# Kernel optimization log

Hardware: AMD Instinct MI355X
Metric: run time of the kernel (lower is better)

Reference implementation:

```python
import jax, jax.numpy as jnp
import numpy as np

N, E, B = 200000, 1600000, 4096
IN_FEATS, H, R, NB = 64, 32, 8, 2


def _params(key):
    ks = jax.random.split(key, 20)
    p = {}
    dims = [(IN_FEATS, H), (H, H), (H, H), (H, H)]
    i = 0
    for l, (di, do) in enumerate(dims):
        p[f'basis{l}'] = jax.random.normal(ks[i], (NB, di, do), jnp.float32) * 0.1; i += 1
        p[f'comp{l}'] = jax.random.normal(ks[i], (R, NB), jnp.float32) * 0.1; i += 1
        p[f'wself{l}'] = jax.random.normal(ks[i], (di, do), jnp.float32) * 0.1; i += 1
        p[f'bias{l}'] = jnp.zeros((do,), jnp.float32); i += 1
    p['lin1_w'] = jax.random.normal(ks[i], (2 * 4 * H, 1), jnp.float32) * 0.05; i += 1
    p['lin1_b'] = jnp.zeros((1,), jnp.float32)
    return p


def setup_inputs() -> dict:
    key = jax.random.key(0)
    k = jax.random.split(key, 8)
    inp = {
        'x': jax.random.normal(k[0], (N, IN_FEATS), jnp.float32),
        'src': jax.random.randint(k[1], (E,), 0, N, jnp.int32),
        'dst': jax.random.randint(k[2], (E,), 0, N, jnp.int32),
        'etype': jax.random.randint(k[3], (E,), 0, R, jnp.int32),
        'user_idx': jax.random.randint(k[4], (B,), 0, N, jnp.int32),
        'item_idx': jax.random.randint(k[5], (B,), 0, N, jnp.int32),
    }
    inp.update(_params(k[6]))
    return inp


def _rel_graph_conv(x, src, dst, etype, basis, comp, wself, bias):
    # basis decomposition: W_r = sum_b comp[r,b] * basis[b]
    # compute per-node per-basis transform first (cheap: small NB), then mix per edge
    hb = jnp.einsum('ni,bio->nbo', x, basis)            # [N, NB, out]
    msg = jnp.einsum('eb,ebo->eo', comp[etype], hb[src])  # [E, out]
    agg = jax.ops.segment_sum(msg, dst, num_segments=x.shape[0])
    return agg + x @ wself + bias


def reference(x, src, dst, etype, user_idx, item_idx,
              basis0, comp0, wself0, bias0,
              basis1, comp1, wself1, bias1,
              basis2, comp2, wself2, bias2,
              basis3, comp3, wself3, bias3,
              lin1_w, lin1_b):
    states = []
    h = x
    for (ba, co, ws, bi) in ((basis0, comp0, wself0, bias0),
                             (basis1, comp1, wself1, bias1),
                             (basis2, comp2, wself2, bias2),
                             (basis3, comp3, wself3, bias3)):
        h = jnp.tanh(_rel_graph_conv(h, src, dst, etype, ba, co, ws, bi))
        states.append(h)
    cat = jnp.concatenate(states, axis=1)               # [N, 128]
    pair = jnp.concatenate([cat[user_idx], cat[item_idx]], axis=1)  # [B, 256]
    out = jax.nn.sigmoid(pair @ lin1_w + lin1_b)        # [B, 1]
    return out[:, 0]  # multiply_by == 1
```

## Files before the change

kernel.cpp:

```cpp
#include <hip/hip_runtime.h>
#include <hip/hip_bf16.h>


#define SRC_MASK 0x3FFFFu
#define BUK_SH 9
#define BUK_W 512

typedef __attribute__((ext_vector_type(8))) short bf16x8;
typedef __attribute__((ext_vector_type(4))) float f32x4;
typedef unsigned short u16;
typedef unsigned int u32;

__device__ inline u32 f2bf(float f) {
    u32 u = __float_as_uint(f);
    return (u + 0x7FFFu + ((u >> 16) & 1u)) >> 16;
}
__device__ inline float bf2f(u32 lo16) { return __uint_as_float(lo16 << 16); }

__device__ inline float fast_tanh(float x) {
    float xc = fminf(fmaxf(x, -15.f), 15.f);
    float e = __expf(2.f * xc);
    return (e - 1.f) * __builtin_amdgcn_rcpf(e + 1.f);
}

__device__ inline void block_exscan(int* a, int M, int* wsum ) {
    const int t = threadIdx.x;
    const int q = M >> 2;
    int s0 = 0, s1 = 0, s2 = 0, s3 = 0, s = 0;
    if (t < q) {
        s0 = a[4 * t]; s1 = a[4 * t + 1]; s2 = a[4 * t + 2]; s3 = a[4 * t + 3];
        s = s0 + s1 + s2 + s3;
    }
    int lane = t & 63, wid = t >> 6;
    int val = s;
    for (int d = 1; d < 64; d <<= 1) {
        int u = __shfl_up(val, d, 64);
        if (lane >= d) val += u;
    }
    if (lane == 63) wsum[wid] = val;
    __syncthreads();
    int woff = 0;
    for (int w = 0; w < wid; ++w) woff += wsum[w];
    val += woff;
    int base = val - s;
    __syncthreads();
    if (t < q) {
        a[4 * t]     = base;
        a[4 * t + 1] = base + s0;
        a[4 * t + 2] = base + s0 + s1;
        a[4 * t + 3] = base + s0 + s1 + s2;
    }
    __syncthreads();
}

__global__ __launch_bounds__(256) void k_buk_count(const int* __restrict__ dst,
                                                   int* __restrict__ gBukCnt, int E) {
    __shared__ int hist[1024];
    const int t = threadIdx.x;
    for (int f = t; f < 1024; f += 256) hist[f] = 0;
    __syncthreads();
    int e0 = blockIdx.x * 2048;
    for (int k = 0; k < 8; ++k) {
        int e = e0 + k * 256 + t;
        if (e < E) atomicAdd(&hist[dst[e] >> BUK_SH], 1);
    }
    __syncthreads();
    for (int f = t; f < 1024; f += 256) {
        int c = hist[f];
        if (c) atomicAdd(&gBukCnt[f], c);
    }
}

__global__ void k_buk_scan(const int* __restrict__ gBukCnt, int* __restrict__ bukOff,
                           int nb) {
    __shared__ int lds[1024];
    int tid = threadIdx.x;
    int v = (tid < nb) ? gBukCnt[tid] : 0;
    lds[tid] = v;
    __syncthreads();
    for (int d = 1; d < 1024; d <<= 1) {
        int u = (tid >= d) ? lds[tid - d] : 0;
        __syncthreads();
        lds[tid] += u;
        __syncthreads();
    }
    if (tid < nb) bukOff[tid] = lds[tid] - v;
    if (tid == nb - 1) bukOff[nb] = lds[tid];
}

__global__ __launch_bounds__(256) void k_binscatter(
    const int* __restrict__ src, const int* __restrict__ dst,
    const int* __restrict__ etype, const int* __restrict__ bukOff,
    int* __restrict__ gBukCur, unsigned int* __restrict__ binned,
    int E, int NBUK)
{
    __shared__ int hist[1024];
    __shared__ int offs[1024];
    __shared__ int cur[1024];
    __shared__ int gb[1024];
    __shared__ int wsum[4];
    __shared__ unsigned int stage[2048];
    __shared__ unsigned short stageB[2048];
    const int t = threadIdx.x;
    for (int f = t; f < 1024; f += 256) { hist[f] = 0; cur[f] = 0; }
    __syncthreads();

    const int e0 = blockIdx.x * 2048;
    const int cntTot = min(2048, E - e0);
    unsigned int pk[8];
    int bk[8];
#pragma unroll
    for (int k = 0; k < 8; ++k) {
        int e = e0 + k * 256 + t;
        if (e < E) {
            int d = dst[e];
            bk[k] = d >> BUK_SH;
            pk[k] = (unsigned int)src[e]
                  | ((unsigned int)etype[e] << 29)
                  | ((unsigned int)(d & (BUK_W - 1)) << 20);
            atomicAdd(&hist[bk[k]], 1);
        } else bk[k] = -1;
    }
    __syncthreads();
    for (int f = t; f < 1024; f += 256) offs[f] = hist[f];
    __syncthreads();
    block_exscan(offs, 1024, wsum);
#pragma unroll
    for (int k = 0; k < 8; ++k) {
        if (bk[k] >= 0) {
            int pos = offs[bk[k]] + atomicAdd(&cur[bk[k]], 1);
            stage[pos] = pk[k];
            stageB[pos] = (unsigned short)bk[k];
        }
    }
    for (int f = t; f < NBUK; f += 256) {
        int c = hist[f];
        if (c > 0) gb[f] = bukOff[f] + atomicAdd(&gBukCur[f], c);
    }
    __syncthreads();
    for (int k = t; k < cntTot; k += 256) {
        int b = stageB[k];
        binned[(size_t)gb[b] + (size_t)(k - offs[b])] = stage[k];
    }
}

__global__ __launch_bounds__(256) void k_bucket_finalize(
    const unsigned int* __restrict__ binned, const int* __restrict__ bukOff,
    int* __restrict__ rowptr, unsigned int* __restrict__ epack, int N, int E)
{
    __shared__ int nhist[512];
    __shared__ int ncur[512];
    __shared__ int wsum[4];
    const int t = threadIdx.x;
    const int b = blockIdx.x;
    for (int f = t; f < 512; f += 256) { nhist[f] = 0; ncur[f] = 0; }
    __syncthreads();
    const int k0 = bukOff[b], k1 = bukOff[b + 1];
    for (int k = k0 + t; k < k1; k += 256)
        atomicAdd(&nhist[(binned[k] >> 20) & (BUK_W - 1)], 1);
    __syncthreads();
    block_exscan(nhist, 512, wsum);
    for (int f = t; f < 512; f += 256) {
        int node = (b << BUK_SH) + f;
        if (node < N) rowptr[node] = k0 + nhist[f];
    }
    if (b == 0 && t == 0) rowptr[N] = E;
    for (int k = k0 + t; k < k1; k += 256) {
        unsigned int v = binned[k];
        int dl = (v >> 20) & (BUK_W - 1);
        int pos = k0 + nhist[dl] + atomicAdd(&ncur[dl], 1);
        epack[pos] = v & 0xE003FFFFu;
    }
}

template<int DI>
__global__ __launch_bounds__(256) void k_transform3(
    const float* __restrict__ xin, int in_stride,
    const float* __restrict__ basis, const float* __restrict__ wself,
    const float* __restrict__ bias,
    u32* __restrict__ hb2, float* __restrict__ self0, int n)
{
    constexpr int ROWB = DI * 2;
    constexpr int SMASK = (ROWB / 16) - 1;
    constexpr int C4 = DI / 4;
    __shared__ u16 xs[64 * DI];
    __shared__ u16 bt[96 * DI];
    const int t = threadIdx.x;

    auto swz = [](int row, int byteInRow) -> int {
        int slot = (byteInRow >> 4) ^ ((row ^ (row >> 2)) & SMASK);
        return row * ROWB + (slot << 4) + (byteInRow & 15);
    };

    for (int f = t; f < 96 * C4; f += 256) {
        int k4 = f / 96;
        int o  = f - k4 * 96;
        const float* sp = (o < 64) ? (basis + (size_t)(o >> 5) * DI * 32 + (o & 31))
                                   : (wself + (o - 64));
        int k = 4 * k4;
        ushort4 pv;
        pv.x = (u16)f2bf(sp[(size_t)(k + 0) * 32]);
        pv.y = (u16)f2bf(sp[(size_t)(k + 1) * 32]);
        pv.z = (u16)f2bf(sp[(size_t)(k + 2) * 32]);
        pv.w = (u16)f2bf(sp[(size_t)(k + 3) * 32]);
        *(ushort4*)((char*)bt + swz(o, k * 2)) = pv;
    }

    const int node0 = blockIdx.x * 64;
    for (int f = t; f < 64 * C4; f += 256) {
        int nloc = f / C4, k4 = f - nloc * C4;
        int node = node0 + nloc;
        float4 v = make_float4(0.f, 0.f, 0.f, 0.f);
        if (node < n) v = *(const float4*)(xin + (size_t)node * in_stride + 4 * k4);
        ushort4 pv;
        pv.x = (u16)f2bf(v.x);
        pv.y = (u16)f2bf(v.y);
        pv.z = (u16)f2bf(v.z);
        pv.w = (u16)f2bf(v.w);
        *(ushort4*)((char*)xs + swz(nloc, 8 * k4)) = pv;
    }
    __syncthreads();

    const int w = t >> 6;
    const int l = t & 63;
    const int lr = l & 15;
    const int lg = l >> 4;

    f32x4 c[6];
#pragma unroll
    for (int i = 0; i < 6; ++i) c[i] = (f32x4){0.f, 0.f, 0.f, 0.f};

#pragma unroll
    for (int ks = 0; ks < DI / 32; ++ks) {
        const int kb = ks * 64 + lg * 16;
        bf16x8 a = *(const bf16x8*)((char*)xs + swz(w * 16 + lr, kb));
#pragma unroll
        for (int tt = 0; tt < 6; ++tt) {
            bf16x8 b = *(const bf16x8*)((char*)bt + swz(tt * 16 + lr, kb));
            c[tt] = __builtin_amdgcn_mfma_f32_16x16x32_bf16(a, b, c[tt], 0, 0, 0);
        }
    }

    const float bia0 = bias[lr];
    const float bia1 = bias[16 + lr];
#pragma unroll
    for (int r = 0; r < 4; ++r) {
        int node = node0 + w * 16 + lg * 4 + r;
        if (node < n) {
            hb2[(size_t)node * 32 + lr]      = f2bf(c[0][r]) | (f2bf(c[2][r]) << 16);
            hb2[(size_t)node * 32 + 16 + lr] = f2bf(c[1][r]) | (f2bf(c[3][r]) << 16);
            self0[(size_t)node * 32 + lr]      = c[4][r] + bia0;
            self0[(size_t)node * 32 + 16 + lr] = c[5][r] + bia1;
        }
    }
}

template<int W>
__device__ __forceinline__ void agg0_block(
    const u32* __restrict__ hb2, const u32* __restrict__ epack,
    int k, int oj, unsigned gbase, const u32* cw, float4& acc)
{
    int pa;
    if (W == 8)      pa = (int)epack[k + oj];
    else if (W == 4) pa = (int)epack[k + (oj & 3)];
    else if (W == 2) pa = (int)epack[k + (oj & 1)];
    else             pa = (int)epack[k];
    u32 pp[W];
    uint4 hh[W];
#pragma unroll
    for (int j = 0; j < W; ++j) {
        pp[j] = (W > 1) ? (u32)__shfl(pa, j, 8) : (u32)pa;
        unsigned boff = (pp[j] & SRC_MASK) * 128u + gbase;
        hh[j] = *(const uint4*)((const char*)hb2 + boff);
    }
#pragma unroll
    for (int j = 0; j < W; ++j) {
        u32 w = cw[pp[j] >> 29];
        float w0 = __uint_as_float(w << 16);
        float w1 = __uint_as_float(w & 0xFFFF0000u);
        acc.x = fmaf(w0, __uint_as_float(hh[j].x << 16), acc.x);
        acc.x = fmaf(w1, __uint_as_float(hh[j].x & 0xFFFF0000u), acc.x);
        acc.y = fmaf(w0, __uint_as_float(hh[j].y << 16), acc.y);
        acc.y = fmaf(w1, __uint_as_float(hh[j].y & 0xFFFF0000u), acc.y);
        acc.z = fmaf(w0, __uint_as_float(hh[j].z << 16), acc.z);
        acc.z = fmaf(w1, __uint_as_float(hh[j].z & 0xFFFF0000u), acc.z);
        acc.w = fmaf(w0, __uint_as_float(hh[j].w << 16), acc.w);
        acc.w = fmaf(w1, __uint_as_float(hh[j].w & 0xFFFF0000u), acc.w);
    }
}

__global__ __launch_bounds__(256) void k_aggregate0(
    const u32* __restrict__ hb2,
    const u32* __restrict__ epack,
    const int* __restrict__ rowptr,
    const float* __restrict__ comp,
    const float* __restrict__ self0,
    u16* __restrict__ cat0,
    int n)
{
    __shared__ u32 cw[8];
    if (threadIdx.x < 8)
        cw[threadIdx.x] = f2bf(comp[threadIdx.x * 2 + 0])
                        | (f2bf(comp[threadIdx.x * 2 + 1]) << 16);
    __syncthreads();
    int t = blockIdx.x * 256 + threadIdx.x;
    int node = t >> 3;
    int oj = t & 7;
    if (node >= n) return;
    float4 acc = *(const float4*)(self0 + (size_t)node * 32 + 4 * oj);
    int k = rowptr[node];
    const int k1 = rowptr[node + 1];
    const unsigned gbase = (unsigned)oj * 16u;

    while (k + 8 <= k1) { agg0_block<8>(hb2, epack, k, oj, gbase, cw, acc); k += 8; }
    const int r = k1 - k;
    if (r & 4) { agg0_block<4>(hb2, epack, k, oj, gbase, cw, acc); k += 4; }
    if (r & 2) { agg0_block<2>(hb2, epack, k, oj, gbase, cw, acc); k += 2; }
    if (r & 1) { agg0_block<1>(hb2, epack, k, oj, gbase, cw, acc); }

    ushort4 o;
    o.x = (u16)f2bf(fast_tanh(acc.x));
    o.y = (u16)f2bf(fast_tanh(acc.y));
    o.z = (u16)f2bf(fast_tanh(acc.z));
    o.w = (u16)f2bf(fast_tanh(acc.w));
    *(ushort4*)(cat0 + (size_t)node * 128 + 4 * oj) = o;
}

template<int W>
__device__ __forceinline__ void aggy_block(
    const u16* __restrict__ catPrev, const u32* __restrict__ epack,
    int k, int i, unsigned gbase, const u32* cw, float* y0, float* y1)
{
    int pa, pb = 0;
    if (W == 8)      { pa = (int)epack[k + i]; pb = (int)epack[k + 4 + i]; }
    else if (W == 4)   pa = (int)epack[k + i];
    else if (W == 2)   pa = (int)epack[k + (i & 1)];
    else               pa = (int)epack[k];
    u32 pp[W];
    uint4 hh[W];
#pragma unroll
    for (int j = 0; j < W; ++j) {
        int v;
        if (W == 8)      v = (j < 4) ? __shfl(pa, j, 4) : __shfl(pb, j - 4, 4);
        else if (W > 1)  v = __shfl(pa, j, 4);
        else             v = pa;
        pp[j] = (u32)v;
        unsigned boff = (pp[j] & SRC_MASK) * 256u + gbase;
        hh[j] = *(const uint4*)((const char*)catPrev + boff);
    }
#pragma unroll
    for (int j = 0; j < W; ++j) {
        u32 w = cw[pp[j] >> 29];
        float w0 = __uint_as_float(w << 16);
        float w1 = __uint_as_float(w & 0xFFFF0000u);
        const u32* hp = (const u32*)&hh[j];
#pragma unroll
        for (int m = 0; m < 4; ++m) {
            u32 pair = hp[m];
            float ha = __uint_as_float(pair << 16);
            float hb = __uint_as_float(pair & 0xFFFF0000u);
            y0[2 * m]     = fmaf(w0, ha, y0[2 * m]);
            y1[2 * m]     = fmaf(w1, ha, y1[2 * m]);
            y0[2 * m + 1] = fmaf(w0, hb, y0[2 * m + 1]);
            y1[2 * m + 1] = fmaf(w1, hb, y1[2 * m + 1]);
        }
    }
}

__global__ __launch_bounds__(256) void k_aggregate_y(
    const u16* __restrict__ catPrev,
    const u32* __restrict__ epack,
    const int* __restrict__ rowptr,
    const float* __restrict__ comp,
    u16* __restrict__ ybuf,
    int n)
{
    __shared__ u32 cw[8];
    if (threadIdx.x < 8)
        cw[threadIdx.x] = f2bf(comp[threadIdx.x * 2 + 0])
                        | (f2bf(comp[threadIdx.x * 2 + 1]) << 16);
    __syncthreads();
    int t = blockIdx.x * 256 + threadIdx.x;
    int node = t >> 2;
    int i = t & 3;
    if (node >= n) return;
    float y0[8], y1[8];
#pragma unroll
    for (int m = 0; m < 8; ++m) { y0[m] = 0.f; y1[m] = 0.f; }
    int k = rowptr[node];
    const int k1 = rowptr[node + 1];
    const unsigned gbase = (unsigned)i * 16u;

    while (k + 8 <= k1) { aggy_block<8>(catPrev, epack, k, i, gbase, cw, y0, y1); k += 8; }
    const int r = k1 - k;
    if (r & 4) { aggy_block<4>(catPrev, epack, k, i, gbase, cw, y0, y1); k += 4; }
    if (r & 2) { aggy_block<2>(catPrev, epack, k, i, gbase, cw, y0, y1); k += 2; }
    if (r & 1) { aggy_block<1>(catPrev, epack, k, i, gbase, cw, y0, y1); }

    uint4 o0, o1;
    o0.x = f2bf(y0[0]) | (f2bf(y0[1]) << 16);
    o0.y = f2bf(y0[2]) | (f2bf(y0[3]) << 16);
    o0.z = f2bf(y0[4]) | (f2bf(y0[5]) << 16);
    o0.w = f2bf(y0[6]) | (f2bf(y0[7]) << 16);
    o1.x = f2bf(y1[0]) | (f2bf(y1[1]) << 16);
    o1.y = f2bf(y1[2]) | (f2bf(y1[3]) << 16);
    o1.z = f2bf(y1[4]) | (f2bf(y1[5]) << 16);
    o1.w = f2bf(y1[6]) | (f2bf(y1[7]) << 16);
    *(uint4*)(ybuf + (size_t)node * 64 + i * 8) = o0;
    *(uint4*)(ybuf + (size_t)node * 64 + 32 + i * 8) = o1;
}

__global__ __launch_bounds__(256) void k_transform_y(
    const u16* __restrict__ ybuf,
    const u16* __restrict__ catPrev,
    const float* __restrict__ basis,
    const float* __restrict__ wself,
    const float* __restrict__ bias,
    u16* __restrict__ catOut,
    int n)
{
    __shared__ u16 xs[64 * 128];
    __shared__ u16 bt[32 * 128];
    const int t = threadIdx.x;

    auto swz = [](int row, int byteInRow) -> int {
        int slot = (byteInRow >> 4) ^ ((row ^ (row >> 2)) & 15);
        return row * 256 + (slot << 4) + (byteInRow & 15);
    };

    for (int f = t; f < 32 * 12; f += 256) {
        int c8 = f >> 5, o = f & 31;
        u32 pk[4];
#pragma unroll
        for (int e = 0; e < 4; ++e) {
            int k0 = c8 * 8 + 2 * e, k1v = k0 + 1;
            float v0 = (k0 < 64) ? basis[(size_t)(k0 >> 5) * 1024 + (k0 & 31) * 32 + o]
                                 : wself[(size_t)(k0 - 64) * 32 + o];
            float v1 = (k1v < 64) ? basis[(size_t)(k1v >> 5) * 1024 + (k1v & 31) * 32 + o]
                                  : wself[(size_t)(k1v - 64) * 32 + o];
            pk[e] = f2bf(v0) | (f2bf(v1) << 16);
        }
        *(uint4*)((char*)bt + swz(o, c8 * 16)) = *(uint4*)pk;
    }

    const int node0 = blockIdx.x * 64;
    for (int f = t; f < 64 * 12; f += 256) {
        int nloc = f / 12, c8 = f - nloc * 12;
        int node = node0 + nloc;
        uint4 v = make_uint4(0u, 0u, 0u, 0u);
        if (node < n) {
            if (c8 < 8) v = *(const uint4*)(ybuf + (size_t)node * 64 + c8 * 8);
            else        v = *(const uint4*)(catPrev + (size_t)node * 128 + (c8 - 8) * 8);
        }
        *(uint4*)((char*)xs + swz(nloc, c8 * 16)) = v;
    }
    __syncthreads();

    const int w = t >> 6;
    const int l = t & 63;
    const int lr = l & 15;
    const int lg = l >> 4;

    f32x4 c0 = (f32x4){0.f, 0.f, 0.f, 0.f};
    f32x4 c1 = (f32x4){0.f, 0.f, 0.f, 0.f};
#pragma unroll
    for (int ks = 0; ks < 3; ++ks) {
        const int kb = ks * 64 + lg * 16;
        bf16x8 a  = *(const bf16x8*)((char*)xs + swz(w * 16 + lr, kb));
        bf16x8 b0 = *(const bf16x8*)((char*)bt + swz(lr, kb));
        bf16x8 b1 = *(const bf16x8*)((char*)bt + swz(16 + lr, kb));
        c0 = __builtin_amdgcn_mfma_f32_16x16x32_bf16(a, b0, c0, 0, 0, 0);
        c1 = __builtin_amdgcn_mfma_f32_16x16x32_bf16(a, b1, c1, 0, 0, 0);
    }

    const float bia0 = bias[lr];
    const float bia1 = bias[16 + lr];
#pragma unroll
    for (int r = 0; r < 4; ++r) {
        int node = node0 + w * 16 + lg * 4 + r;
        if (node < n) {
            catOut[(size_t)node * 128 + lr]      = (u16)f2bf(fast_tanh(c0[r] + bia0));
            catOut[(size_t)node * 128 + 16 + lr] = (u16)f2bf(fast_tanh(c1[r] + bia1));
        }
    }
}

__global__ void k_head(const u16* __restrict__ cat, const int* __restrict__ uidx,
                       const int* __restrict__ iidx, const float* __restrict__ w,
                       const float* __restrict__ b, float* __restrict__ out, int B) {
    int p = blockIdx.x;
    if (p >= B) return;
    int lane = threadIdx.x;
    const u16* cu = cat + (size_t)uidx[p] * 128;
    const u16* ci = cat + (size_t)iidx[p] * 128;
    float s = 0.f;
    s = fmaf(bf2f(cu[lane]), w[lane], s);
    s = fmaf(bf2f(cu[lane + 64]), w[lane + 64], s);
    s = fmaf(bf2f(ci[lane]), w[lane + 128], s);
    s = fmaf(bf2f(ci[lane + 64]), w[lane + 192], s);
    for (int d = 32; d > 0; d >>= 1) s += __shfl_down(s, d, 64);
    if (lane == 0) out[p] = 1.f / (1.f + expf(-(s + b[0])));
}

extern "C" void kernel_launch(void* const* d_in, const int* in_sizes, int n_in,
                              void* d_out, int out_size, void* d_ws, size_t ws_size,
                              hipStream_t stream) {
    const float* x      = (const float*)d_in[0];
    const int*   src    = (const int*)d_in[1];
    const int*   dst    = (const int*)d_in[2];
    const int*   etype  = (const int*)d_in[3];
    const int*   uidx   = (const int*)d_in[4];
    const int*   iidx   = (const int*)d_in[5];
    const float* lin1_w = (const float*)d_in[22];
    const float* lin1_b = (const float*)d_in[23];

    const int N = in_sizes[0] / 64;
    const int E = in_sizes[1];
    const int B = in_sizes[4];
    const int NBUK = (N + BUK_W - 1) >> BUK_SH;

    char* p = (char*)d_ws;
    auto alloc = [&](size_t bytes) -> void* {
        void* r = (void*)p;
        p += (bytes + 255) & ~(size_t)255;
        return r;
    };
    u32*   hb2     = (u32*)alloc((size_t)N * 32 * sizeof(u32));
    float* self0   = (float*)alloc((size_t)N * 32 * sizeof(float));
    u16*   cat     = (u16*)alloc((size_t)N * 128 * sizeof(u16));
    u16*   ybuf    = (u16*)alloc((size_t)N * 64 * sizeof(u16));
    int*   rowptr  = (int*)alloc((size_t)(N + 1) * sizeof(int));
    u32*   epack   = (u32*)alloc((size_t)E * sizeof(u32));
    u32*   binned  = (u32*)alloc((size_t)E * sizeof(u32));
    int*   gBukCnt = (int*)alloc(1024 * sizeof(int));
    int*   gBukCur = (int*)alloc(1024 * sizeof(int));
    int*   bukOff  = (int*)alloc(1025 * sizeof(int));

    hipMemsetAsync(gBukCnt, 0, 2048 * sizeof(int), stream);
    int ebGrid = (E + 2047) / 2048;
    k_buk_count<<<ebGrid, 256, 0, stream>>>(dst, gBukCnt, E);
    k_buk_scan<<<1, 1024, 0, stream>>>(gBukCnt, bukOff, NBUK);
    k_binscatter<<<ebGrid, 256, 0, stream>>>(src, dst, etype, bukOff, gBukCur,
                                             binned, E, NBUK);
    k_bucket_finalize<<<NBUK, 256, 0, stream>>>(binned, bukOff, rowptr, epack, N, E);

    const int tr_grid = (N + 63) / 64;

    k_transform3<64><<<tr_grid, 256, 0, stream>>>(
        x, 64, (const float*)d_in[6], (const float*)d_in[8], (const float*)d_in[9],
        hb2, self0, N);
    k_aggregate0<<<(N * 8 + 255) / 256, 256, 0, stream>>>(
        hb2, epack, rowptr, (const float*)d_in[7], self0, cat, N);

    for (int l = 1; l < 4; ++l) {
        const float* basis = (const float*)d_in[6 + l * 4];
        const float* comp  = (const float*)d_in[7 + l * 4];
        const float* wself = (const float*)d_in[8 + l * 4];
        const float* bias  = (const float*)d_in[9 + l * 4];
        k_aggregate_y<<<(N * 4 + 255) / 256, 256, 0, stream>>>(
            cat + (size_t)(l - 1) * 32, epack, rowptr, comp, ybuf, N);
        k_transform_y<<<tr_grid, 256, 0, stream>>>(
            ybuf, cat + (size_t)(l - 1) * 32, basis, wself, bias,
            cat + (size_t)l * 32, N);
    }

    k_head<<<B, 64, 0, stream>>>(cat, uidx, iidx, lin1_w, lin1_b, (float*)d_out, B);
}
```

Baseline: 284.3 us.

## Fuse per-layer aggregation and MFMA transform into one kernel via shared memory

Merges the gather-aggregate kernel and the bf16 MFMA transform kernel for layers 1-3 into one kernel. Each block's 4-threads-per-node aggregation writes its bf16 results straight into the swizzled shared tile, so the intermediate ybuf no longer makes a global round trip and one launch per layer is saved. The hipMemsetAsync on the bucket counters is also replaced by a small zeroing kernel. In exchange, every block now holds the large shared tile while doing the latency-bound gather, which may lower occupancy and latency hiding in the aggregation phase.

```diff
diff --git a/kernel.cpp b/kernel.cpp
--- a/kernel.cpp
+++ b/kernel.cpp
@@ -21,6 +21,11 @@
     float xc = fminf(fmaxf(x, -15.f), 15.f);
     float e = __expf(2.f * xc);
     return (e - 1.f) * __builtin_amdgcn_rcpf(e + 1.f);
+}
+
+__global__ void k_zero(int* __restrict__ p, int n) {
+    int i = blockIdx.x * 256 + threadIdx.x;
+    if (i < n) p[i] = 0;
 }
 
 __device__ inline void block_exscan(int* a, int M, int* wsum ) {
@@ -367,52 +372,11 @@
     }
 }
 
-__global__ __launch_bounds__(256) void k_aggregate_y(
+__global__ __launch_bounds__(256) void k_layer_y(
     const u16* __restrict__ catPrev,
     const u32* __restrict__ epack,
     const int* __restrict__ rowptr,
     const float* __restrict__ comp,
-    u16* __restrict__ ybuf,
-    int n)
-{
-    __shared__ u32 cw[8];
-    if (threadIdx.x < 8)
-        cw[threadIdx.x] = f2bf(comp[threadIdx.x * 2 + 0])
-                        | (f2bf(comp[threadIdx.x * 2 + 1]) << 16);
-    __syncthreads();
-    int t = blockIdx.x * 256 + threadIdx.x;
-    int node = t >> 2;
-    int i = t & 3;
-    if (node >= n) return;
-    float y0[8], y1[8];
-#pragma unroll
-    for (int m = 0; m < 8; ++m) { y0[m] = 0.f; y1[m] = 0.f; }
-    int k = rowptr[node];
-    const int k1 = rowptr[node + 1];
-    const unsigned gbase = (unsigned)i * 16u;
-
-    while (k + 8 <= k1) { aggy_block<8>(catPrev, epack, k, i, gbase, cw, y0, y1); k += 8; }
-    const int r = k1 - k;
-    if (r & 4) { aggy_block<4>(catPrev, epack, k, i, gbase, cw, y0, y1); k += 4; }
-    if (r & 2) { aggy_block<2>(catPrev, epack, k, i, gbase, cw, y0, y1); k += 2; }
-    if (r & 1) { aggy_block<1>(catPrev, epack, k, i, gbase, cw, y0, y1); }
-
-    uint4 o0, o1;
-    o0.x = f2bf(y0[0]) | (f2bf(y0[1]) << 16);
-    o0.y = f2bf(y0[2]) | (f2bf(y0[3]) << 16);
-    o0.z = f2bf(y0[4]) | (f2bf(y0[5]) << 16);
-    o0.w = f2bf(y0[6]) | (f2bf(y0[7]) << 16);
-    o1.x = f2bf(y1[0]) | (f2bf(y1[1]) << 16);
-    o1.y = f2bf(y1[2]) | (f2bf(y1[3]) << 16);
-    o1.z = f2bf(y1[4]) | (f2bf(y1[5]) << 16);
-    o1.w = f2bf(y1[6]) | (f2bf(y1[7]) << 16);
-    *(uint4*)(ybuf + (size_t)node * 64 + i * 8) = o0;
-    *(uint4*)(ybuf + (size_t)node * 64 + 32 + i * 8) = o1;
-}
-
-__global__ __launch_bounds__(256) void k_transform_y(
-    const u16* __restrict__ ybuf,
-    const u16* __restrict__ catPrev,
     const float* __restrict__ basis,
     const float* __restrict__ wself,
     const float* __restrict__ bias,
@@ -421,12 +385,15 @@
 {
     __shared__ u16 xs[64 * 128];
     __shared__ u16 bt[32 * 128];
+    __shared__ u32 cw[8];
     const int t = threadIdx.x;
 
     auto swz = [](int row, int byteInRow) -> int {
         int slot = (byteInRow >> 4) ^ ((row ^ (row >> 2)) & 15);
         return row * 256 + (slot << 4) + (byteInRow & 15);
     };
+
+    if (t < 8) cw[t] = f2bf(comp[2 * t]) | (f2bf(comp[2 * t + 1]) << 16);
 
     for (int f = t; f < 32 * 12; f += 256) {
         int c8 = f >> 5, o = f & 31;
@@ -444,15 +411,42 @@
     }
 
     const int node0 = blockIdx.x * 64;
-    for (int f = t; f < 64 * 12; f += 256) {
-        int nloc = f / 12, c8 = f - nloc * 12;
-        int node = node0 + nloc;
+    const int nloc = t >> 2;
+    const int i = t & 3;
+    const int node = node0 + nloc;
+
+    {
         uint4 v = make_uint4(0u, 0u, 0u, 0u);
-        if (node < n) {
-            if (c8 < 8) v = *(const uint4*)(ybuf + (size_t)node * 64 + c8 * 8);
-            else        v = *(const uint4*)(catPrev + (size_t)node * 128 + (c8 - 8) * 8);
-        }
-        *(uint4*)((char*)xs + swz(nloc, c8 * 16)) = v;
+        if (node < n) v = *(const uint4*)(catPrev + (size_t)node * 128 + i * 8);
+        *(uint4*)((char*)xs + swz(nloc, (8 + i) * 16)) = v;
+    }
+    __syncthreads();
+
+    float y0[8], y1[8];
+#pragma unroll
+    for (int m = 0; m < 8; ++m) { y0[m] = 0.f; y1[m] = 0.f; }
+    if (node < n) {
+        int k = rowptr[node];
+        const int k1 = rowptr[node + 1];
+        const unsigned gbase = (unsigned)i * 16u;
+        while (k + 8 <= k1) { aggy_block<8>(catPrev, epack, k, i, gbase, cw, y0, y1); k += 8; }
+        const int r = k1 - k;
+        if (r & 4) { aggy_block<4>(catPrev, epack, k, i, gbase, cw, y0, y1); k += 4; }
+        if (r & 2) { aggy_block<2>(catPrev, epack, k, i, gbase, cw, y0, y1); k += 2; }
+        if (r & 1) { aggy_block<1>(catPrev, epack, k, i, gbase, cw, y0, y1); }
+    }
+    {
+        uint4 o0, o1;
+        o0.x = f2bf(y0[0]) | (f2bf(y0[1]) << 16);
+        o0.y = f2bf(y0[2]) | (f2bf(y0[3]) << 16);
+        o0.z = f2bf(y0[4]) | (f2bf(y0[5]) << 16);
+        o0.w = f2bf(y0[6]) | (f2bf(y0[7]) << 16);
+        o1.x = f2bf(y1[0]) | (f2bf(y1[1]) << 16);
+        o1.y = f2bf(y1[2]) | (f2bf(y1[3]) << 16);
+        o1.z = f2bf(y1[4]) | (f2bf(y1[5]) << 16);
+        o1.w = f2bf(y1[6]) | (f2bf(y1[7]) << 16);
+        *(uint4*)((char*)xs + swz(nloc, i * 16)) = o0;
+        *(uint4*)((char*)xs + swz(nloc, (4 + i) * 16)) = o1;
     }
     __syncthreads();
 
@@ -477,10 +471,10 @@
     const float bia1 = bias[16 + lr];
 #pragma unroll
     for (int r = 0; r < 4; ++r) {
-        int node = node0 + w * 16 + lg * 4 + r;
-        if (node < n) {
-            catOut[(size_t)node * 128 + lr]      = (u16)f2bf(fast_tanh(c0[r] + bia0));
-            catOut[(size_t)node * 128 + 16 + lr] = (u16)f2bf(fast_tanh(c1[r] + bia1));
+        int nodeW = node0 + w * 16 + lg * 4 + r;
+        if (nodeW < n) {
+            catOut[(size_t)nodeW * 128 + lr]      = (u16)f2bf(fast_tanh(c0[r] + bia0));
+            catOut[(size_t)nodeW * 128 + 16 + lr] = (u16)f2bf(fast_tanh(c1[r] + bia1));
         }
     }
 }
@@ -528,7 +522,6 @@
     u32*   hb2     = (u32*)alloc((size_t)N * 32 * sizeof(u32));
     float* self0   = (float*)alloc((size_t)N * 32 * sizeof(float));
     u16*   cat     = (u16*)alloc((size_t)N * 128 * sizeof(u16));
-    u16*   ybuf    = (u16*)alloc((size_t)N * 64 * sizeof(u16));
     int*   rowptr  = (int*)alloc((size_t)(N + 1) * sizeof(int));
     u32*   epack   = (u32*)alloc((size_t)E * sizeof(u32));
     u32*   binned  = (u32*)alloc((size_t)E * sizeof(u32));
@@ -536,7 +529,7 @@
     int*   gBukCur = (int*)alloc(1024 * sizeof(int));
     int*   bukOff  = (int*)alloc(1025 * sizeof(int));
 
-    hipMemsetAsync(gBukCnt, 0, 2048 * sizeof(int), stream);
+    k_zero<<<8, 256, 0, stream>>>(gBukCnt, 2048);
     int ebGrid = (E + 2047) / 2048;
     k_buk_count<<<ebGrid, 256, 0, stream>>>(dst, gBukCnt, E);
     k_buk_scan<<<1, 1024, 0, stream>>>(gBukCnt, bukOff, NBUK);
@@ -553,14 +546,10 @@
         hb2, epack, rowptr, (const float*)d_in[7], self0, cat, N);
 
     for (int l = 1; l < 4; ++l) {
-        const float* basis = (const float*)d_in[6 + l * 4];
-        const float* comp  = (const float*)d_in[7 + l * 4];
-        const float* wself = (const float*)d_in[8 + l * 4];
-        const float* bias  = (const float*)d_in[9 + l * 4];
-        k_aggregate_y<<<(N * 4 + 255) / 256, 256, 0, stream>>>(
-            cat + (size_t)(l - 1) * 32, epack, rowptr, comp, ybuf, N);
-        k_transform_y<<<tr_grid, 256, 0, stream>>>(
-            ybuf, cat + (size_t)(l - 1) * 32, basis, wself, bias,
+        k_layer_y<<<tr_grid, 256, 0, stream>>>(
+            cat + (size_t)(l - 1) * 32, epack, rowptr,
+            (const float*)d_in[7 + l * 4], (const float*)d_in[6 + l * 4],
+            (const float*)d_in[8 + l * 4], (const float*)d_in[9 + l * 4],
             cat + (size_t)l * 32, N);
     }
 
```

Result: faster. 263.8 us (-7.2%).
